# Optimization experiments

Hardware: AMD Instinct MI355X
Metric: run time of the kernel (lower is better)

The kernel has to match this reference:

```python
import jax, jax.numpy as jnp
import numpy as np

B, N, DIM = 4, 2048, 1024
HEADS, DIM_HEAD = 16, 64
HIDDEN = HEADS * DIM_HEAD  # 1024
SCALE = 1.0 / np.sqrt(DIM_HEAD).astype(np.float32)


def setup_inputs() -> dict:
    key = jax.random.key(0)
    k1, k2, k3 = jax.random.split(key, 3)
    x = jax.random.normal(k1, (B, N, DIM), dtype=jnp.float32)
    # Linear(dim, 3*hidden, bias=False): stored as [in, out] for x @ W
    w_qkv = jax.random.normal(k2, (DIM, 3 * HIDDEN), dtype=jnp.float32) * (1.0 / np.sqrt(DIM))
    w_out = jax.random.normal(k3, (HIDDEN, DIM), dtype=jnp.float32) * (1.0 / np.sqrt(HIDDEN))
    b_out = jnp.zeros((DIM,), dtype=jnp.float32)
    return {"x": x, "w_qkv": w_qkv, "w_out": w_out, "b_out": b_out}


def reference(x, w_qkv, w_out, b_out):
    b, n, _ = x.shape
    qkv = x @ w_qkv                                  # [b, n, 3*hidden]
    q, k, v = jnp.split(qkv, 3, axis=-1)             # each [b, n, hidden]

    def to_heads(t):
        return t.reshape(b, n, HEADS, DIM_HEAD).transpose(0, 2, 1, 3)  # [b, h, n, d]

    q, k, v = to_heads(q), to_heads(k), to_heads(v)
    scores = jnp.einsum('bhid,bhjd->bhij', q, k) * SCALE   # [b, h, n_q, n_k]
    # Faithful to original: softmax over dim=2 (the QUERY axis), not keys.
    attn = jax.nn.softmax(scores, axis=2)
    y = jnp.einsum('bhij,bhjd->bhid', attn, v)             # [b, h, n, d]
    y = y.transpose(0, 2, 1, 3).reshape(b, n, HIDDEN)      # [b, n, hidden]
    return y @ w_out + b_out
```

## Files before the change

kernel.cpp:

```cpp
#include <hip/hip_runtime.h>
#include <math.h>
#include <stdint.h>

#define B_    4
#define N_    2048
#define DIM_  1024
#define H_    16
#define DH_   64
#define HID_  1024
#define RS_   3072
#define C2_   0.1803368801111204f

typedef unsigned short u16;
typedef unsigned int   u32;
typedef short  bf16x8 __attribute__((ext_vector_type(8)));
typedef u16    u16x8  __attribute__((ext_vector_type(8)));
typedef float  f32x4  __attribute__((ext_vector_type(4)));
typedef float  f32x16 __attribute__((ext_vector_type(16)));

__device__ inline u16 f2b(float x) {
    u32 u = __float_as_uint(x);
    return (u16)((u + 0x7fffu + ((u >> 16) & 1u)) >> 16);
}
__device__ inline float b2f(u16 x) {
    return __uint_as_float((u32)x << 16);
}

__device__ inline u32 pack2bf(float f0, float f1) {
    u32 u0 = __float_as_uint(f0) + 0x8000u;
    u32 u1 = __float_as_uint(f1) + 0x8000u;
    return __builtin_amdgcn_perm(u1, u0, 0x07060302u);
}

#if defined(__has_builtin)
#if __has_builtin(__builtin_amdgcn_global_load_lds)
#define USE_GLL 1
#endif
#endif

#ifdef USE_GLL
typedef const __attribute__((address_space(1))) u32* gas_ptr;
typedef __attribute__((address_space(3))) u32* las_ptr;
__device__ inline void gll16(const void* g, void* l) {
    __builtin_amdgcn_global_load_lds((gas_ptr)g, (las_ptr)l, 16, 0, 0);
}
#endif

__global__ __launch_bounds__(256) void cast_bf16(const float* __restrict__ in,
                                                 u16* __restrict__ out, int n) {
    int i = (blockIdx.x * 256 + threadIdx.x) * 8;
    if (i >= n) return;
    float4 a = *(const float4*)&in[i];
    float4 b = *(const float4*)&in[i + 4];
    u16x8 p;
    p[0] = f2b(a.x); p[1] = f2b(a.y); p[2] = f2b(a.z); p[3] = f2b(a.w);
    p[4] = f2b(b.x); p[5] = f2b(b.y); p[6] = f2b(b.z); p[7] = f2b(b.w);
    *(u16x8*)&out[i] = p;
}

__global__ __launch_bounds__(256) void transpose_cast(const float* __restrict__ W,
                                                      u16* __restrict__ Wt,
                                                      int K, int Nn, int qcols) {
    __shared__ float t[64][65];
    const int tid = threadIdx.x;
    const int k0 = blockIdx.y * 64, n0 = blockIdx.x * 64;
    for (int idx = tid; idx < 64 * 16; idx += 256) {
        int r = idx >> 4, c4 = (idx & 15) * 4;
        float4 g = *(const float4*)&W[(size_t)(k0 + r) * Nn + n0 + c4];
        t[r][c4] = g.x; t[r][c4 + 1] = g.y; t[r][c4 + 2] = g.z; t[r][c4 + 3] = g.w;
    }
    __syncthreads();
    for (int idx = tid; idx < 64 * 8; idx += 256) {
        int n = idx >> 3, k8 = (idx & 7) * 8;
        float s = (n0 + n < qcols) ? C2_ : 1.0f;
        u16x8 p;
        #pragma unroll
        for (int u = 0; u < 8; u++) p[u] = f2b(t[k8 + u][n] * s);
        *(u16x8*)&Wt[(size_t)(n0 + n) * K + k0 + k8] = p;
    }
}

__global__ __launch_bounds__(256) void build_vT(const u16* __restrict__ qkvb,
                                                const float* __restrict__ invl,
                                                u16* __restrict__ vT) {
    __shared__ u16 t[64 * 72];
    __shared__ float li[64];
    const int tid = threadIdx.x;
    const int bh = blockIdx.y, b = bh >> 4, h = bh & 15;
    const int j0 = blockIdx.x * 64;
    const u16* vbase = qkvb + (size_t)b * N_ * RS_ + 2 * HID_ + h * DH_;
    for (int idx = tid; idx < 512; idx += 256) {
        int r = idx >> 3, d8 = (idx & 7) * 8;
        *(u16x8*)&t[r * 72 + d8] = *(const u16x8*)&vbase[(size_t)(j0 + r) * RS_ + d8];
    }
    if (tid < 64) li[tid] = invl[(size_t)bh * N_ + j0 + tid];
    __syncthreads();
    {
        int d = tid >> 2, j16 = (tid & 3) * 16;
        u16x8 p0, p1;
        #pragma unroll
        for (int u = 0; u < 8; u++) {
            p0[u] = f2b(b2f(t[(j16 + u) * 72 + d]) * li[j16 + u]);
            p1[u] = f2b(b2f(t[(j16 + 8 + u) * 72 + d]) * li[j16 + 8 + u]);
        }
        size_t o = ((size_t)bh * DH_ + d) * N_ + j0 + j16;
        *(u16x8*)&vT[o] = p0;
        *(u16x8*)&vT[o + 8] = p1;
    }
}

template<int BF16OUT>
__global__ __launch_bounds__(256) void gemm_bt(const u16* __restrict__ A,
                                               const u16* __restrict__ Bt,
                                               const float* __restrict__ bias,
                                               void* __restrict__ Cout,
                                               int M, int Nn, int K) {
    __shared__ u16 at[128 * 32];
    __shared__ u16 bt[128 * 32];
    const int tid = threadIdx.x;
    const int lane = tid & 63, wave = tid >> 6;
    const int wr = wave >> 1, wc = wave & 1;
    const int mlane = lane & 15, quad = lane >> 4;
    const int m0 = blockIdx.y * 128, n0 = blockIdx.x * 128;
    const int r = tid >> 2, kc = (tid & 3) * 8;

    f32x4 acc[4][4] = {};

    for (int k0 = 0; k0 < K; k0 += 32) {
        __syncthreads();
#ifdef USE_GLL
        gll16(&A[(size_t)(m0 + r) * K + k0 + kc],       &at[r * 32 + kc]);
        gll16(&A[(size_t)(m0 + r + 64) * K + k0 + kc],  &at[(r + 64) * 32 + kc]);
        gll16(&Bt[(size_t)(n0 + r) * K + k0 + kc],      &bt[r * 32 + kc]);
        gll16(&Bt[(size_t)(n0 + r + 64) * K + k0 + kc], &bt[(r + 64) * 32 + kc]);
#else
        *(u16x8*)&at[r * 32 + kc]        = *(const u16x8*)&A[(size_t)(m0 + r) * K + k0 + kc];
        *(u16x8*)&at[(r + 64) * 32 + kc] = *(const u16x8*)&A[(size_t)(m0 + r + 64) * K + k0 + kc];
        *(u16x8*)&bt[r * 32 + kc]        = *(const u16x8*)&Bt[(size_t)(n0 + r) * K + k0 + kc];
        *(u16x8*)&bt[(r + 64) * 32 + kc] = *(const u16x8*)&Bt[(size_t)(n0 + r + 64) * K + k0 + kc];
#endif
        __syncthreads();

        bf16x8 af[4], bf[4];
        #pragma unroll
        for (int rt = 0; rt < 4; rt++)
            af[rt] = *(const bf16x8*)&at[(wr * 64 + rt * 16 + mlane) * 32 + quad * 8];
        #pragma unroll
        for (int ct = 0; ct < 4; ct++)
            bf[ct] = *(const bf16x8*)&bt[(wc * 64 + ct * 16 + mlane) * 32 + quad * 8];
        #pragma unroll
        for (int rt = 0; rt < 4; rt++)
            #pragma unroll
            for (int ct = 0; ct < 4; ct++)
                acc[rt][ct] = __builtin_amdgcn_mfma_f32_16x16x32_bf16(af[rt], bf[ct], acc[rt][ct], 0, 0, 0);
    }

    const int row0 = m0 + wr * 64 + quad * 4;
    const int col0 = n0 + wc * 64 + mlane;
    #pragma unroll
    for (int rt = 0; rt < 4; rt++)
        #pragma unroll
        for (int ct = 0; ct < 4; ct++) {
            int c = col0 + ct * 16;
            float bv = (!BF16OUT && bias != nullptr) ? bias[c] : 0.f;
            #pragma unroll
            for (int reg = 0; reg < 4; reg++) {
                int rr = row0 + rt * 16 + reg;
                float v = acc[rt][ct][reg] + bv;
                if (BF16OUT) ((u16*)Cout)[(size_t)rr * Nn + c] = f2b(v);
                else         ((float*)Cout)[(size_t)rr * Nn + c] = v;
            }
        }
}

__global__ __launch_bounds__(256) void attn_stats(const u16* __restrict__ qkvb,
                                                  float* __restrict__ invl) {
    __shared__ u16 kt[64 * 72];
    __shared__ u16 qt[4][64 * 72];
    __shared__ float red[4][64];

    const int tid = threadIdx.x;
    const int lane = tid & 63, wave = tid >> 6;
    const int mlane = lane & 15, quad = lane >> 4;
    const int bh = blockIdx.y, b = bh >> 4, h = bh & 15;
    const int j0 = blockIdx.x * 64;

    const u16* qbase = qkvb + (size_t)b * N_ * RS_ + h * DH_;
    const u16* kbase = qbase + HID_;

    for (int idx = tid; idx < 512; idx += 256) {
        int r = idx >> 3, d8 = (idx & 7) * 8;
        *(u16x8*)&kt[r * 72 + d8] = *(const u16x8*)&kbase[(size_t)(j0 + r) * RS_ + d8];
    }
    __syncthreads();

    bf16x8 kf[4][2];
    #pragma unroll
    for (int t = 0; t < 4; t++)
        #pragma unroll
        for (int ks = 0; ks < 2; ks++)
            kf[t][ks] = *(const bf16x8*)&kt[(t * 16 + mlane) * 72 + ks * 32 + quad * 8];

    f32x4 acc[4] = {};
    u16* qw = &qt[wave][0];

    const int prr = lane >> 3, pd8 = (lane & 7) * 8;
    u16x8 pq[8];
    #pragma unroll
    for (int t = 0; t < 8; t++)
        pq[t] = *(const u16x8*)&qbase[(size_t)(wave * 64 + t * 8 + prr) * RS_ + pd8];

    for (int i0 = wave * 64; i0 < N_; i0 += 256) {
        #pragma unroll
        for (int t = 0; t < 8; t++)
            *(u16x8*)&qw[(t * 8 + prr) * 72 + pd8] = pq[t];
        int in = i0 + 256;
        if (in < N_) {
            #pragma unroll
            for (int t = 0; t < 8; t++)
                pq[t] = *(const u16x8*)&qbase[(size_t)(in + t * 8 + prr) * RS_ + pd8];
        }
        #pragma unroll
        for (int q4 = 0; q4 < 4; q4++) {
            bf16x8 bq0 = *(const bf16x8*)&qw[(q4 * 16 + mlane) * 72 + quad * 8];
            bf16x8 bq1 = *(const bf16x8*)&qw[(q4 * 16 + mlane) * 72 + 32 + quad * 8];
            #pragma unroll
            for (int t = 0; t < 4; t++) {
                f32x4 z = {0.f, 0.f, 0.f, 0.f};
                z = __builtin_amdgcn_mfma_f32_16x16x32_bf16(kf[t][0], bq0, z, 0, 0, 0);
                z = __builtin_amdgcn_mfma_f32_16x16x32_bf16(kf[t][1], bq1, z, 0, 0, 0);
                #pragma unroll
                for (int reg = 0; reg < 4; reg++)
                    acc[t][reg] += __builtin_amdgcn_exp2f(z[reg]);
            }
        }
    }

    #pragma unroll
    for (int t = 0; t < 4; t++)
        #pragma unroll
        for (int reg = 0; reg < 4; reg++) {
            float v = acc[t][reg];
            v += __shfl_xor(v, 1, 64);
            v += __shfl_xor(v, 2, 64);
            v += __shfl_xor(v, 4, 64);
            v += __shfl_xor(v, 8, 64);
            if (mlane == 0) red[wave][t * 16 + quad * 4 + reg] = v;
        }
    __syncthreads();
    if (tid < 64) {
        float l = red[0][tid] + red[1][tid] + red[2][tid] + red[3][tid];
        invl[(size_t)bh * N_ + j0 + tid] = 1.0f / l;
    }
}

__global__ __launch_bounds__(256) void attn_apply(const u16* __restrict__ qkvb,
                                                  const u16* __restrict__ vT,
                                                  u16* __restrict__ yb) {
    __shared__ u16 S[256 * 72];

    const int tid = threadIdx.x;
    const int lane = tid & 63, wave = tid >> 6;
    const int m31 = lane & 31, half = lane >> 5;
    const int bh = blockIdx.y, b = bh >> 4, h = bh & 15;
    const int i0 = blockIdx.x * 256;

    const u16* qbase = qkvb + (size_t)b * N_ * RS_ + h * DH_;
    const u16* kbase = qbase + HID_;
    const u16* vbase = vT + (size_t)bh * DH_ * N_;

    for (int idx = tid; idx < 2048; idx += 256) {
        int r = idx >> 3, d8 = (idx & 7) * 8;
        *(u16x8*)&S[r * 72 + d8] = *(const u16x8*)&qbase[(size_t)(i0 + r) * RS_ + d8];
    }
    __syncthreads();

    bf16x8 qf[2][4];
    #pragma unroll
    for (int qc = 0; qc < 2; qc++)
        #pragma unroll
        for (int ks = 0; ks < 4; ks++)
            qf[qc][ks] = *(const bf16x8*)&S[(wave * 64 + qc * 32 + m31) * 72 + ks * 16 + half * 8];

    const int pr = tid >> 3, pc8 = (tid & 7) * 8;
    u16x8 pk0, pk1, pv0, pv1;
    pk0 = *(const u16x8*)&kbase[(size_t)pr * RS_ + pc8];
    pk1 = *(const u16x8*)&kbase[(size_t)(pr + 32) * RS_ + pc8];
    pv0 = *(const u16x8*)&vbase[(size_t)pr * N_ + pc8];
    pv1 = *(const u16x8*)&vbase[(size_t)(pr + 32) * N_ + pc8];

    f32x16 yacc[2][2] = {};

    for (int j0 = 0; j0 < N_; j0 += 64) {
        __syncthreads();
        *(u16x8*)&S[pr * 72 + pc8]        = pk0;
        *(u16x8*)&S[(pr + 32) * 72 + pc8] = pk1;
        *(u16x8*)&S[(pr + 64) * 72 + pc8] = pv0;
        *(u16x8*)&S[(pr + 96) * 72 + pc8] = pv1;
        __syncthreads();

        int jn = j0 + 64;
        if (jn < N_) {
            pk0 = *(const u16x8*)&kbase[(size_t)(jn + pr) * RS_ + pc8];
            pk1 = *(const u16x8*)&kbase[(size_t)(jn + pr + 32) * RS_ + pc8];
            pv0 = *(const u16x8*)&vbase[(size_t)pr * N_ + jn + pc8];
            pv1 = *(const u16x8*)&vbase[(size_t)(pr + 32) * N_ + jn + pc8];
        }

        bf16x8 pa[2][4];
        #pragma unroll
        for (int kt = 0; kt < 2; kt++) {
            bf16x8 ka[4];
            #pragma unroll
            for (int ks = 0; ks < 4; ks++)
                ka[ks] = *(const bf16x8*)&S[(kt * 32 + m31) * 72 + ks * 16 + half * 8];

            f32x16 sc[2] = {};
            #pragma unroll
            for (int ks = 0; ks < 4; ks++)
                #pragma unroll
                for (int qc = 0; qc < 2; qc++)
                    sc[qc] = __builtin_amdgcn_mfma_f32_32x32x16_bf16(ka[ks], qf[qc][ks], sc[qc], 0, 0, 0);

            #pragma unroll
            for (int qc = 0; qc < 2; qc++) {
                u32 U[4][2];
                #pragma unroll
                for (int rb = 0; rb < 4; rb++)
                    #pragma unroll
                    for (int pp = 0; pp < 2; pp++) {
                        float e0 = __builtin_amdgcn_exp2f(sc[qc][4 * rb + 2 * pp]);
                        float e1 = __builtin_amdgcn_exp2f(sc[qc][4 * rb + 2 * pp + 1]);
                        U[rb][pp] = pack2bf(e0, e1);
                    }
                #pragma unroll
                for (int ksl = 0; ksl < 2; ksl++) {
                    const int rb0 = 2 * ksl;
                    u32 a0 = U[rb0][0], a1 = U[rb0][1];
                    u32 b0 = U[rb0 + 1][0], b1 = U[rb0 + 1][1];
                    u32 e0 = half ? a0 : b0, e1 = half ? a1 : b1;
                    u32 g0 = (u32)__shfl_xor((int)e0, 32, 64);
                    u32 g1 = (u32)__shfl_xor((int)e1, 32, 64);
                    u32 o0 = half ? b0 : a0, o1 = half ? b1 : a1;
                    union { u32 u[4]; bf16x8 v; } cv;
                    cv.u[0] = half ? g0 : o0;
                    cv.u[1] = half ? g1 : o1;
                    cv.u[2] = half ? o0 : g0;
                    cv.u[3] = half ? o1 : g1;
                    pa[qc][2 * kt + ksl] = cv.v;
                }
            }
        }

        #pragma unroll
        for (int ks16 = 0; ks16 < 4; ks16++) {
            bf16x8 vb0 = *(const bf16x8*)&S[(64 + m31) * 72 + ks16 * 16 + half * 8];
            bf16x8 vb1 = *(const bf16x8*)&S[(96 + m31) * 72 + ks16 * 16 + half * 8];
            #pragma unroll
            for (int qc = 0; qc < 2; qc++) {
                yacc[qc][0] = __builtin_amdgcn_mfma_f32_32x32x16_bf16(pa[qc][ks16], vb0, yacc[qc][0], 0, 0, 0);
                yacc[qc][1] = __builtin_amdgcn_mfma_f32_32x32x16_bf16(pa[qc][ks16], vb1, yacc[qc][1], 0, 0, 0);
            }
        }
    }

    #pragma unroll
    for (int qc = 0; qc < 2; qc++)
        #pragma unroll
        for (int dt = 0; dt < 2; dt++)
            #pragma unroll
            for (int reg = 0; reg < 16; reg++) {
                int q = i0 + wave * 64 + qc * 32 + (reg & 3) + 8 * (reg >> 2) + 4 * half;
                yb[((size_t)b * N_ + q) * HID_ + h * DH_ + dt * 32 + m31] = f2b(yacc[qc][dt][reg]);
            }
}

extern "C" void kernel_launch(void* const* d_in, const int* in_sizes, int n_in,
                              void* d_out, int out_size, void* d_ws, size_t ws_size,
                              hipStream_t stream) {
    (void)in_sizes; (void)n_in; (void)out_size; (void)ws_size;

    const float* x     = (const float*)d_in[0];
    const float* w_qkv = (const float*)d_in[1];
    const float* w_out = (const float*)d_in[2];
    const float* b_out = (const float*)d_in[3];

    u16* xb    = (u16*)d_ws;
    u16* wqkvT = xb    + (size_t)8192 * 1024;
    u16* woutT = wqkvT + (size_t)3072 * 1024;
    u16* qkvb  = woutT + (size_t)1024 * 1024;
    u16* vTb   = qkvb  + (size_t)8192 * 3072;
    u16* yb    = vTb   + (size_t)64 * 64 * 2048;
    float* invl = (float*)(yb + (size_t)8192 * 1024);

    cast_bf16<<<4096, 256, 0, stream>>>(x, xb, 8192 * 1024);
    transpose_cast<<<dim3(3072 / 64, 1024 / 64), 256, 0, stream>>>(w_qkv, wqkvT, 1024, 3072, HID_);
    transpose_cast<<<dim3(1024 / 64, 1024 / 64), 256, 0, stream>>>(w_out, woutT, 1024, 1024, 0);

    gemm_bt<1><<<dim3(3072 / 128, 8192 / 128), 256, 0, stream>>>(
        xb, wqkvT, nullptr, qkvb, 8192, 3072, 1024);

    attn_stats<<<dim3(N_ / 64, 64), 256, 0, stream>>>(qkvb, invl);
    build_vT<<<dim3(N_ / 64, 64), 256, 0, stream>>>(qkvb, invl, vTb);
    attn_apply<<<dim3(N_ / 256, 64), 256, 0, stream>>>(qkvb, vTb, yb);

    gemm_bt<0><<<dim3(1024 / 128, 8192 / 128), 256, 0, stream>>>(
        yb, woutT, b_out, d_out, 8192, 1024, 1024);
}
```

Baseline: 357.6 us.

## Fuse attention column stats with V transpose and remap block IDs for XCD locality

Folds the build_vT kernel into attn_stats, so the reciprocal column sums stay in shared memory and V is scaled and transposed in the same block. This drops one launch and the invl round trip through global memory. Both GEMMs and the fused kernel now use a 1D grid whose block index is remapped so that consecutive IDs (likely dispatched round-robin across the 8 XCDs) land on tiles sharing A rows or the same head, which is meant to improve L2 reuse. The kt buffer is reused for V after a barrier.

```diff
diff --git a/kernel.cpp b/kernel.cpp
--- a/kernel.cpp
+++ b/kernel.cpp
@@ -77,35 +77,6 @@
         #pragma unroll
         for (int u = 0; u < 8; u++) p[u] = f2b(t[k8 + u][n] * s);
         *(u16x8*)&Wt[(size_t)(n0 + n) * K + k0 + k8] = p;
-    }
-}
-
-__global__ __launch_bounds__(256) void build_vT(const u16* __restrict__ qkvb,
-                                                const float* __restrict__ invl,
-                                                u16* __restrict__ vT) {
-    __shared__ u16 t[64 * 72];
-    __shared__ float li[64];
-    const int tid = threadIdx.x;
-    const int bh = blockIdx.y, b = bh >> 4, h = bh & 15;
-    const int j0 = blockIdx.x * 64;
-    const u16* vbase = qkvb + (size_t)b * N_ * RS_ + 2 * HID_ + h * DH_;
-    for (int idx = tid; idx < 512; idx += 256) {
-        int r = idx >> 3, d8 = (idx & 7) * 8;
-        *(u16x8*)&t[r * 72 + d8] = *(const u16x8*)&vbase[(size_t)(j0 + r) * RS_ + d8];
-    }
-    if (tid < 64) li[tid] = invl[(size_t)bh * N_ + j0 + tid];
-    __syncthreads();
-    {
-        int d = tid >> 2, j16 = (tid & 3) * 16;
-        u16x8 p0, p1;
-        #pragma unroll
-        for (int u = 0; u < 8; u++) {
-            p0[u] = f2b(b2f(t[(j16 + u) * 72 + d]) * li[j16 + u]);
-            p1[u] = f2b(b2f(t[(j16 + 8 + u) * 72 + d]) * li[j16 + 8 + u]);
-        }
-        size_t o = ((size_t)bh * DH_ + d) * N_ + j0 + j16;
-        *(u16x8*)&vT[o] = p0;
-        *(u16x8*)&vT[o + 8] = p1;
     }
 }
 
@@ -121,7 +92,10 @@
     const int lane = tid & 63, wave = tid >> 6;
     const int wr = wave >> 1, wc = wave & 1;
     const int mlane = lane & 15, quad = lane >> 4;
-    const int m0 = blockIdx.y * 128, n0 = blockIdx.x * 128;
+    const int id = blockIdx.x;
+    const int mt = (id & 7) * 8 + ((id >> 3) & 7);
+    const int nt = id >> 6;
+    const int m0 = mt * 128, n0 = nt * 128;
     const int r = tid >> 2, kc = (tid & 3) * 8;
 
     f32x4 acc[4][4] = {};
@@ -173,20 +147,24 @@
         }
 }
 
-__global__ __launch_bounds__(256) void attn_stats(const u16* __restrict__ qkvb,
-                                                  float* __restrict__ invl) {
+__global__ __launch_bounds__(256) void attn_stats_vt(const u16* __restrict__ qkvb,
+                                                     u16* __restrict__ vT) {
     __shared__ u16 kt[64 * 72];
     __shared__ u16 qt[4][64 * 72];
     __shared__ float red[4][64];
+    __shared__ float li[64];
 
     const int tid = threadIdx.x;
     const int lane = tid & 63, wave = tid >> 6;
     const int mlane = lane & 15, quad = lane >> 4;
-    const int bh = blockIdx.y, b = bh >> 4, h = bh & 15;
-    const int j0 = blockIdx.x * 64;
+    const int id = blockIdx.x;
+    const int bh = (id & 7) * 8 + ((id >> 3) & 7);
+    const int b = bh >> 4, h = bh & 15;
+    const int j0 = (id >> 6) * 64;
 
     const u16* qbase = qkvb + (size_t)b * N_ * RS_ + h * DH_;
     const u16* kbase = qbase + HID_;
+    const u16* vbase = qbase + 2 * HID_;
 
     for (int idx = tid; idx < 512; idx += 256) {
         int r = idx >> 3, d8 = (idx & 7) * 8;
@@ -250,7 +228,25 @@
     __syncthreads();
     if (tid < 64) {
         float l = red[0][tid] + red[1][tid] + red[2][tid] + red[3][tid];
-        invl[(size_t)bh * N_ + j0 + tid] = 1.0f / l;
+        li[tid] = 1.0f / l;
+    }
+
+    for (int idx = tid; idx < 512; idx += 256) {
+        int r = idx >> 3, d8 = (idx & 7) * 8;
+        *(u16x8*)&kt[r * 72 + d8] = *(const u16x8*)&vbase[(size_t)(j0 + r) * RS_ + d8];
+    }
+    __syncthreads();
+    {
+        int d = tid >> 2, j16 = (tid & 3) * 16;
+        u16x8 p0, p1;
+        #pragma unroll
+        for (int u = 0; u < 8; u++) {
+            p0[u] = f2b(b2f(kt[(j16 + u) * 72 + d]) * li[j16 + u]);
+            p1[u] = f2b(b2f(kt[(j16 + 8 + u) * 72 + d]) * li[j16 + 8 + u]);
+        }
+        size_t o = ((size_t)bh * DH_ + d) * N_ + j0 + j16;
+        *(u16x8*)&vT[o] = p0;
+        *(u16x8*)&vT[o + 8] = p1;
     }
 }
 
@@ -391,19 +387,18 @@
     u16* qkvb  = woutT + (size_t)1024 * 1024;
     u16* vTb   = qkvb  + (size_t)8192 * 3072;
     u16* yb    = vTb   + (size_t)64 * 64 * 2048;
-    float* invl = (float*)(yb + (size_t)8192 * 1024);
 
     cast_bf16<<<4096, 256, 0, stream>>>(x, xb, 8192 * 1024);
     transpose_cast<<<dim3(3072 / 64, 1024 / 64), 256, 0, stream>>>(w_qkv, wqkvT, 1024, 3072, HID_);
     transpose_cast<<<dim3(1024 / 64, 1024 / 64), 256, 0, stream>>>(w_out, woutT, 1024, 1024, 0);
 
-    gemm_bt<1><<<dim3(3072 / 128, 8192 / 128), 256, 0, stream>>>(
+    gemm_bt<1><<<64 * 24, 256, 0, stream>>>(
         xb, wqkvT, nullptr, qkvb, 8192, 3072, 1024);
 
-    attn_stats<<<dim3(N_ / 64, 64), 256, 0, stream>>>(qkvb, invl);
-    build_vT<<<dim3(N_ / 64, 64), 256, 0, stream>>>(qkvb, invl, vTb);
+    attn_stats_vt<<<32 * 64, 256, 0, stream>>>(qkvb, vTb);
+
     attn_apply<<<dim3(N_ / 256, 64), 256, 0, stream>>>(qkvb, vTb, yb);
 
-    gemm_bt<0><<<dim3(1024 / 128, 8192 / 128), 256, 0, stream>>>(
+    gemm_bt<0><<<64 * 8, 256, 0, stream>>>(
         yb, woutT, b_out, d_out, 8192, 1024, 1024);
 }
```

New measurement: 350.4 us. 2.0% less time.
